# Kernel tuning notes

Measured on AMD Instinct MI355X. Metric: run time of the kernel, lower is better.

The kernel has to match this reference:

```python
import jax, jax.numpy as jnp
import numpy as np

N_NODES = 50000
N_EDGES = 800000
NUM_GRAPHS = 4
IN_DIM, HID_DIM, OUT_DIM = 1024, 128, 1
MAX_RISK = 5.0


def gcn_conv(x, W, b, src, dst, n):
    """PyG GCNConv: add self-loops, sym-normalize, gather-GEMM-scatter."""
    loop = jnp.arange(n, dtype=src.dtype)
    s = jnp.concatenate([src, loop])
    d = jnp.concatenate([dst, loop])
    deg = jax.ops.segment_sum(jnp.ones_like(d, dtype=x.dtype), d, num_segments=n)
    dinv = jnp.where(deg > 0, jax.lax.rsqrt(deg), 0.0)
    norm = dinv[s] * dinv[d]  # [E+N]
    xw = x @ W                # dense GEMM first (fewer FLOPs than per-edge)
    msg = xw[s] * norm[:, None]          # irregular gather, [E+N, out]
    out = jax.ops.segment_sum(msg, d, num_segments=n)  # scatter-add
    return out + b


def setup_inputs() -> dict:
    key = jax.random.key(0)
    ks = jax.random.split(key, 12)
    x = jax.random.normal(ks[0], (N_NODES, IN_DIM), dtype=jnp.float32)
    edge_index = jax.random.randint(ks[1], (2, N_EDGES), 0, N_NODES, dtype=jnp.int64)
    batch = jnp.sort(jax.random.randint(ks[2], (N_NODES,), 0, NUM_GRAPHS, dtype=jnp.int64))

    def glorot(k, fan_in, fan_out):
        s = np.sqrt(6.0 / (fan_in + fan_out)).astype(np.float32)
        return jax.random.uniform(k, (fan_in, fan_out), jnp.float32, -s, s)

    params = {
        'W0': glorot(ks[3], IN_DIM, HID_DIM),  'b0': jnp.zeros((HID_DIM,), jnp.float32),
        'W1': glorot(ks[4], HID_DIM, HID_DIM), 'b1': jnp.zeros((HID_DIM,), jnp.float32),
        'W2': glorot(ks[5], HID_DIM, HID_DIM), 'b2': jnp.zeros((HID_DIM,), jnp.float32),
        'Wl1': glorot(ks[6], 2 * HID_DIM, HID_DIM), 'bl1': jnp.zeros((HID_DIM,), jnp.float32),
        'Wl2': glorot(ks[7], HID_DIM, HID_DIM // 2), 'bl2': jnp.zeros((HID_DIM // 2,), jnp.float32),
        'Wl3': glorot(ks[8], HID_DIM // 2, OUT_DIM), 'bl3': jnp.zeros((OUT_DIM,), jnp.float32),
    }
    return dict(x=x, edge_index=edge_index, batch=batch, **params)


def reference(x, edge_index, batch, W0, b0, W1, b1, W2, b2, Wl1, bl1, Wl2, bl2, Wl3, bl3):
    n = x.shape[0]
    src, dst = edge_index[0], edge_index[1]
    h = jax.nn.relu(gcn_conv(x, W0, b0, src, dst, n))
    h = jax.nn.relu(gcn_conv(h, W1, b1, src, dst, n))
    h = jax.nn.relu(gcn_conv(h, W2, b2, src, dst, n))
    # global max pool + global mean pool per graph
    gmax = jax.ops.segment_max(h, batch, num_segments=NUM_GRAPHS)
    gsum = jax.ops.segment_sum(h, batch, num_segments=NUM_GRAPHS)
    cnt = jax.ops.segment_sum(jnp.ones((n,), h.dtype), batch, num_segments=NUM_GRAPHS)
    gmean = gsum / jnp.maximum(cnt, 1.0)[:, None]
    g = jnp.concatenate([gmax, gmean], axis=1)  # [G, 2*hid]
    g = jax.nn.relu(g @ Wl1 + bl1)
    g = jax.nn.relu(g @ Wl2 + bl2)
    out = g @ Wl3 + bl3
    return jnp.minimum(out, MAX_RISK)
```

## Files before the change

### kernel.cpp

```cpp
#include <hip/hip_runtime.h>
#include <math.h>

#define HID 128
#define NGRAPH 4

typedef int idx_t;
typedef float f32x4 __attribute__((ext_vector_type(4)));
typedef _Float16 h8 __attribute__((ext_vector_type(8)));

__global__ __launch_bounds__(256) void k_count(const idx_t* __restrict__ dst,
                                               int* __restrict__ cnt, int E) {
  int e = blockIdx.x * 256 + threadIdx.x;
  if (e < E) atomicAdd(&cnt[dst[e]], 1);
}

#define SC 1024
__global__ __launch_bounds__(256) void k_scan1(const int* __restrict__ cnt,
                                               int* __restrict__ bsum, int n) {
  __shared__ int sh[256];
  int base = blockIdx.x * SC + threadIdx.x * 4;
  int s = 0;
#pragma unroll
  for (int j = 0; j < 4; ++j) { int i = base + j; if (i < n) s += cnt[i]; }
  sh[threadIdx.x] = s;
  __syncthreads();
  for (int o = 128; o > 0; o >>= 1) {
    if (threadIdx.x < o) sh[threadIdx.x] += sh[threadIdx.x + o];
    __syncthreads();
  }
  if (threadIdx.x == 0) bsum[blockIdx.x] = sh[0];
}

__global__ __launch_bounds__(64) void k_scan2(const int* __restrict__ bsum,
                                              int* __restrict__ boff,
                                              int* __restrict__ off, int nb, int n) {
  int lane = threadIdx.x;
  int v = (lane < nb) ? bsum[lane] : 0;
  for (int d = 1; d < 64; d <<= 1) {
    int t = __shfl_up(v, d);
    if (lane >= d) v += t;
  }
  int ex = __shfl_up(v, 1);
  if (lane == 0) ex = 0;
  if (lane < nb) boff[lane] = ex;
  if (lane == nb - 1) off[n] = v;
}

__global__ __launch_bounds__(256) void k_scan3(const int* __restrict__ cnt,
                                               const int* __restrict__ boff,
                                               int* __restrict__ off,
                                               float* __restrict__ dinv, int n) {
  __shared__ int sh[256];
  int base = blockIdx.x * SC + threadIdx.x * 4;
  int c[4];
  int s = 0;
#pragma unroll
  for (int j = 0; j < 4; ++j) {
    int i = base + j;
    c[j] = (i < n) ? cnt[i] : 0;
    s += c[j];
  }
  sh[threadIdx.x] = s;
  __syncthreads();
  for (int o = 1; o < 256; o <<= 1) {
    int t = (threadIdx.x >= (unsigned)o) ? sh[threadIdx.x - o] : 0;
    __syncthreads();
    sh[threadIdx.x] += t;
    __syncthreads();
  }
  int ex = sh[threadIdx.x] - s + boff[blockIdx.x];
#pragma unroll
  for (int j = 0; j < 4; ++j) {
    int i = base + j;
    if (i < n) {
      off[i] = ex;
      dinv[i] = 1.0f / sqrtf((float)c[j] + 1.0f);
      ex += c[j];
    }
  }
}

__global__ __launch_bounds__(256) void k_fill(const idx_t* __restrict__ src,
                                              const idx_t* __restrict__ dst,
                                              const int* __restrict__ off,
                                              const float* __restrict__ dinv,
                                              int* __restrict__ fillc,
                                              int2* __restrict__ edata, int E) {
  int e = blockIdx.x * 256 + threadIdx.x;
  if (e < E) {
    int s = src[e], d = dst[e];
    int p = atomicAdd(&fillc[d], 1);
    float w = dinv[s] * dinv[d];
    edata[off[d] + p] = make_int2(s, __float_as_int(w));
  }
}

__global__ __launch_bounds__(256) void k_wsplit(const float* __restrict__ W,
                                                _Float16* __restrict__ Wh,
                                                _Float16* __restrict__ Wl, int K) {
  int i = blockIdx.x * 256 + threadIdx.x;
  if (i >= K * HID) return;
  int k = i >> 7, n = i & 127;
  float f = W[i];
  _Float16 h = (_Float16)f;
  Wh[(size_t)n * K + k] = h;
  Wl[(size_t)n * K + k] = (_Float16)(f - (float)h);
}

template <int K, bool F32>
__global__ __launch_bounds__(64) void k_gemm4(const void* __restrict__ Xv,
                                              const _Float16* __restrict__ Wh,
                                              const _Float16* __restrict__ Wl,
                                              _Float16* __restrict__ Y16, int M) {
  const int lane = threadIdx.x & 63;
  const int lrow = lane & 15, kg = lane >> 4;
  const int row0 = blockIdx.x * 32;
  const int ra = row0 + lrow, rb = row0 + 16 + lrow;
  const int rca = (ra < M) ? ra : 0, rcb = (rb < M) ? rb : 0;
  const float* xf0 = (const float*)Xv + (size_t)rca * K + kg * 8;
  const float* xf1 = (const float*)Xv + (size_t)rcb * K + kg * 8;
  const _Float16* xg0 = (const _Float16*)Xv + (size_t)rca * K + kg * 8;
  const _Float16* xg1 = (const _Float16*)Xv + (size_t)rcb * K + kg * 8;
  const _Float16* bh_p = Wh + (size_t)lrow * K + kg * 8;
  const _Float16* bl_p = Wl + (size_t)lrow * K + kg * 8;

  f32x4 acc[2][8] = {};

  for (int k0 = 0; k0 < K; k0 += 32) {
    h8 ah0, al0, ah1, al1;
    if (F32) {
      float4 a0 = *(const float4*)(xf0 + k0);
      float4 a1 = *(const float4*)(xf0 + k0 + 4);
      float4 a2 = *(const float4*)(xf1 + k0);
      float4 a3 = *(const float4*)(xf1 + k0 + 4);
      float t0[8] = {a0.x, a0.y, a0.z, a0.w, a1.x, a1.y, a1.z, a1.w};
      float t1[8] = {a2.x, a2.y, a2.z, a2.w, a3.x, a3.y, a3.z, a3.w};
#pragma unroll
      for (int j = 0; j < 8; ++j) {
        _Float16 h0 = (_Float16)t0[j], h1 = (_Float16)t1[j];
        ah0[j] = h0; al0[j] = (_Float16)(t0[j] - (float)h0);
        ah1[j] = h1; al1[j] = (_Float16)(t1[j] - (float)h1);
      }
    } else {
      ah0 = *(const h8*)(xg0 + k0);
      ah1 = *(const h8*)(xg1 + k0);
    }
#pragma unroll
    for (int ni = 0; ni < 8; ++ni) {
      h8 bh = *(const h8*)(bh_p + (size_t)ni * 16 * K + k0);
      h8 bl = *(const h8*)(bl_p + (size_t)ni * 16 * K + k0);
      acc[0][ni] = __builtin_amdgcn_mfma_f32_16x16x32_f16(ah0, bh, acc[0][ni], 0, 0, 0);
      acc[1][ni] = __builtin_amdgcn_mfma_f32_16x16x32_f16(ah1, bh, acc[1][ni], 0, 0, 0);
      if (F32) {
        acc[0][ni] = __builtin_amdgcn_mfma_f32_16x16x32_f16(al0, bh, acc[0][ni], 0, 0, 0);
        acc[1][ni] = __builtin_amdgcn_mfma_f32_16x16x32_f16(al1, bh, acc[1][ni], 0, 0, 0);
      }
      acc[0][ni] = __builtin_amdgcn_mfma_f32_16x16x32_f16(ah0, bl, acc[0][ni], 0, 0, 0);
      acc[1][ni] = __builtin_amdgcn_mfma_f32_16x16x32_f16(ah1, bl, acc[1][ni], 0, 0, 0);
    }
  }
#pragma unroll
  for (int mi = 0; mi < 2; ++mi)
#pragma unroll
    for (int ni = 0; ni < 8; ++ni)
#pragma unroll
      for (int rr = 0; rr < 4; ++rr) {
        int grow = row0 + mi * 16 + kg * 4 + rr;
        if (grow < M)
          Y16[(size_t)grow * HID + ni * 16 + lrow] = (_Float16)acc[mi][ni][rr];
      }
}

__global__ __launch_bounds__(256) void k_agg16(const _Float16* __restrict__ xh,
                                               const float* __restrict__ dinv,
                                               const int* __restrict__ off,
                                               const int2* __restrict__ edata,
                                               const float* __restrict__ bias,
                                               _Float16* __restrict__ hout, int n) {
  int v = blockIdx.x * 4 + (threadIdx.x >> 6);
  if (v >= n) return;
  int lane = threadIdx.x & 63;
  int grp = lane >> 3, gl = lane & 7;
  int fb = gl * 16;
  float acc[16] = {0.f, 0.f, 0.f, 0.f, 0.f, 0.f, 0.f, 0.f,
                   0.f, 0.f, 0.f, 0.f, 0.f, 0.f, 0.f, 0.f};
  int j0 = off[v], j1 = off[v + 1];
  for (int j = j0 + grp; j < j1; j += 8) {
    int2 e = edata[j];
    float w = __int_as_float(e.y);
    h8 m0 = *(const h8*)&xh[(size_t)e.x * HID + fb];
    h8 m1 = *(const h8*)&xh[(size_t)e.x * HID + fb + 8];
#pragma unroll
    for (int q = 0; q < 8; ++q) {
      acc[q] = fmaf(w, (float)m0[q], acc[q]);
      acc[8 + q] = fmaf(w, (float)m1[q], acc[8 + q]);
    }
  }
#pragma unroll
  for (int q = 0; q < 16; ++q) {
    acc[q] += __shfl_xor(acc[q], 8);
    acc[q] += __shfl_xor(acc[q], 16);
    acc[q] += __shfl_xor(acc[q], 32);
  }
  if (grp == 0) {
    float dv = dinv[v], dv2 = dv * dv;
    h8 s0 = *(const h8*)&xh[(size_t)v * HID + fb];
    h8 s1 = *(const h8*)&xh[(size_t)v * HID + fb + 8];
    h8 o0, o1;
#pragma unroll
    for (int q = 0; q < 8; ++q) {
      float a0 = fmaxf(fmaf(dv2, (float)s0[q], acc[q]) + bias[fb + q], 0.f);
      float a1 = fmaxf(fmaf(dv2, (float)s1[q], acc[8 + q]) + bias[fb + 8 + q], 0.f);
      o0[q] = (_Float16)a0;
      o1[q] = (_Float16)a1;
    }
    *(h8*)&hout[(size_t)v * HID + fb] = o0;
    *(h8*)&hout[(size_t)v * HID + fb + 8] = o1;
  }
}

__global__ __launch_bounds__(256) void k_gcnt(const idx_t* __restrict__ batch,
                                              int* __restrict__ gcnt, int n) {
  __shared__ int h[NGRAPH];
  int tid = threadIdx.x;
  if (tid < NGRAPH) h[tid] = 0;
  __syncthreads();
  int i = blockIdx.x * 256 + tid;
  if (i < n) atomicAdd(&h[batch[i]], 1);
  __syncthreads();
  if (tid < NGRAPH && h[tid]) atomicAdd(&gcnt[tid], h[tid]);
}

__global__ __launch_bounds__(128) void k_pool(const _Float16* __restrict__ h,
                                              const idx_t* __restrict__ batch,
                                              float* __restrict__ gmax,
                                              float* __restrict__ gsum, int n) {
  int f = threadIdx.x;
  int v0 = blockIdx.x * 128;
  int cur = -1;
  float mx = 0.f, sm = 0.f;
  for (int i = 0; i < 128; ++i) {
    int v = v0 + i;
    if (v >= n) break;
    int g = batch[v];
    if (g != cur) {
      if (cur >= 0) {
        atomicMax((int*)&gmax[cur * HID + f], __float_as_int(mx));
        atomicAdd(&gsum[cur * HID + f], sm);
      }
      cur = g; mx = 0.f; sm = 0.f;
    }
    float val = (float)h[(size_t)v * HID + f];
    mx = fmaxf(mx, val);
    sm += val;
  }
  if (cur >= 0) {
    atomicMax((int*)&gmax[cur * HID + f], __float_as_int(mx));
    atomicAdd(&gsum[cur * HID + f], sm);
  }
}

__global__ __launch_bounds__(256) void k_mlp(const float* __restrict__ gmax,
                                             const float* __restrict__ gsum,
                                             const int* __restrict__ gcnt,
                                             const float* __restrict__ Wl1,
                                             const float* __restrict__ bl1,
                                             const float* __restrict__ Wl2,
                                             const float* __restrict__ bl2,
                                             const float* __restrict__ Wl3,
                                             const float* __restrict__ bl3,
                                             float* __restrict__ out) {
  __shared__ float G[NGRAPH][2 * HID];
  __shared__ float H1[NGRAPH][HID];
  __shared__ float H2[NGRAPH][HID / 2];
  int t = threadIdx.x;
  for (int i = t; i < NGRAPH * 2 * HID; i += 256) {
    int gi = i >> 8, j = i & 255;
    float val;
    if (j < HID) val = gmax[gi * HID + j];
    else val = gsum[gi * HID + (j - HID)] / fmaxf((float)gcnt[gi], 1.0f);
    G[gi][j] = val;
  }
  __syncthreads();
  for (int i = t; i < NGRAPH * HID; i += 256) {
    int gi = i >> 7, j = i & 127;
    float a = bl1[j];
    for (int k = 0; k < 2 * HID; ++k) a = fmaf(G[gi][k], Wl1[k * HID + j], a);
    H1[gi][j] = fmaxf(a, 0.f);
  }
  __syncthreads();
  {
    int gi = t >> 6, j = t & 63;
    float a = bl2[j];
    for (int k = 0; k < HID; ++k) a = fmaf(H1[gi][k], Wl2[k * 64 + j], a);
    H2[gi][j] = fmaxf(a, 0.f);
  }
  __syncthreads();
  if (t < NGRAPH) {
    float a = bl3[0];
    for (int k = 0; k < 64; ++k) a = fmaf(H2[t][k], Wl3[k], a);
    out[t] = fminf(a, 5.0f);
  }
}

extern "C" void kernel_launch(void* const* d_in, const int* in_sizes, int n_in,
                              void* d_out, int out_size, void* d_ws, size_t ws_size,
                              hipStream_t stream) {
  const float* x   = (const float*)d_in[0];
  const idx_t* ei  = (const idx_t*)d_in[1];
  const idx_t* bat = (const idx_t*)d_in[2];
  const float* W0 = (const float*)d_in[3];  const float* b0 = (const float*)d_in[4];
  const float* W1 = (const float*)d_in[5];  const float* b1 = (const float*)d_in[6];
  const float* W2 = (const float*)d_in[7];  const float* b2 = (const float*)d_in[8];
  const float* Wl1 = (const float*)d_in[9];  const float* bl1 = (const float*)d_in[10];
  const float* Wl2 = (const float*)d_in[11]; const float* bl2 = (const float*)d_in[12];
  const float* Wl3 = (const float*)d_in[13]; const float* bl3 = (const float*)d_in[14];
  float* out = (float*)d_out;

  const int N = in_sizes[2];
  const int E = in_sizes[1] / 2;
  const idx_t* srcv = ei;
  const idx_t* dstv = ei + E;
  const int nb = (N + SC - 1) / SC;

  char* ws = (char*)d_ws;
  size_t o = 0;
  auto alloc = [&](size_t bytes) -> void* {
    void* p = ws + o;
    o = (o + bytes + 255) & ~(size_t)255;
    return p;
  };
  _Float16* xh  = (_Float16*)alloc((size_t)N * HID * 2);
  _Float16* h16 = (_Float16*)alloc((size_t)N * HID * 2);
  float* dinv = (float*)alloc((size_t)N * 4);
  int* cnt    = (int*)alloc((size_t)N * 4);
  int* off    = (int*)alloc((size_t)(N + 1) * 4);
  int* fillc  = (int*)alloc((size_t)N * 4);
  int2* edata = (int2*)alloc((size_t)E * 8);
  int* bsum   = (int*)alloc(64 * 4);
  int* boff   = (int*)alloc(64 * 4);
  _Float16* Wh0 = (_Float16*)alloc((size_t)1024 * HID * 2);
  _Float16* Wl0 = (_Float16*)alloc((size_t)1024 * HID * 2);
  _Float16* Wh1 = (_Float16*)alloc((size_t)HID * HID * 2);
  _Float16* Wlo1 = (_Float16*)alloc((size_t)HID * HID * 2);
  _Float16* Wh2 = (_Float16*)alloc((size_t)HID * HID * 2);
  _Float16* Wlo2 = (_Float16*)alloc((size_t)HID * HID * 2);
  float* gmax = (float*)alloc(NGRAPH * HID * 4);
  float* gsum = (float*)alloc(NGRAPH * HID * 4);
  int* gcnt   = (int*)alloc(NGRAPH * 4);

  hipMemsetAsync(cnt, 0, (size_t)N * 4, stream);
  hipMemsetAsync(fillc, 0, (size_t)N * 4, stream);
  hipMemsetAsync(gmax, 0, NGRAPH * HID * 4, stream);
  hipMemsetAsync(gsum, 0, NGRAPH * HID * 4, stream);
  hipMemsetAsync(gcnt, 0, NGRAPH * 4, stream);

  k_wsplit<<<(1024 * HID + 255) / 256, 256, 0, stream>>>(W0, Wh0, Wl0, 1024);
  k_wsplit<<<(HID * HID + 255) / 256, 256, 0, stream>>>(W1, Wh1, Wlo1, HID);
  k_wsplit<<<(HID * HID + 255) / 256, 256, 0, stream>>>(W2, Wh2, Wlo2, HID);

  k_count<<<(E + 255) / 256, 256, 0, stream>>>(dstv, cnt, E);
  k_scan1<<<nb, 256, 0, stream>>>(cnt, bsum, N);
  k_scan2<<<1, 64, 0, stream>>>(bsum, boff, off, nb, N);
  k_scan3<<<nb, 256, 0, stream>>>(cnt, boff, off, dinv, N);
  k_fill<<<(E + 255) / 256, 256, 0, stream>>>(srcv, dstv, off, dinv, fillc, edata, E);

  const int gblk = (N + 31) / 32;
  const int ablk = (N + 3) / 4;
  k_gemm4<1024, true><<<gblk, 64, 0, stream>>>(x, Wh0, Wl0, xh, N);
  k_agg16<<<ablk, 256, 0, stream>>>(xh, dinv, off, edata, b0, h16, N);
  k_gemm4<HID, false><<<gblk, 64, 0, stream>>>(h16, Wh1, Wlo1, xh, N);
  k_agg16<<<ablk, 256, 0, stream>>>(xh, dinv, off, edata, b1, h16, N);
  k_gemm4<HID, false><<<gblk, 64, 0, stream>>>(h16, Wh2, Wlo2, xh, N);
  k_agg16<<<ablk, 256, 0, stream>>>(xh, dinv, off, edata, b2, h16, N);

  k_gcnt<<<(N + 255) / 256, 256, 0, stream>>>(bat, gcnt, N);
  k_pool<<<(N + 127) / 128, 128, 0, stream>>>(h16, bat, gmax, gsum, N);
  k_mlp<<<1, 256, 0, stream>>>(gmax, gsum, gcnt, Wl1, bl1, Wl2, bl2, Wl3, bl3, out);
}
```

Before: 451.7 us.

## Split GEMM K across four waves with LDS reduction and fragment-packed weights

The GEMM kernel now uses 256-thread blocks where each of four waves handles a quarter of the K dimension for the same 32-row tile, and the partial sums are combined in shared memory. Weights are pre-packed into MFMA fragment order so each lane's B load is contiguous, and the output is written as 16-byte vector stores. The aim is more parallelism per tile and better-coalesced weight and output traffic. The cost is a serialized four-step LDS reduction with barriers and extra shared-memory use per block.

```diff
diff --git a/kernel.cpp b/kernel.cpp
--- a/kernel.cpp
+++ b/kernel.cpp
@@ -95,44 +95,49 @@
   }
 }
 
-__global__ __launch_bounds__(256) void k_wsplit(const float* __restrict__ W,
-                                                _Float16* __restrict__ Wh,
-                                                _Float16* __restrict__ Wl, int K) {
+__global__ __launch_bounds__(256) void k_wsplitf(const float* __restrict__ W,
+                                                 _Float16* __restrict__ Wh,
+                                                 _Float16* __restrict__ Wl, int K) {
   int i = blockIdx.x * 256 + threadIdx.x;
   if (i >= K * HID) return;
-  int k = i >> 7, n = i & 127;
-  float f = W[i];
+  int j = i & 7, lane = (i >> 3) & 63, ni = (i >> 9) & 7, t = i >> 12;
+  int k = t * 32 + (lane >> 4) * 8 + j;
+  int col = ni * 16 + (lane & 15);
+  float f = W[(size_t)k * HID + col];
   _Float16 h = (_Float16)f;
-  Wh[(size_t)n * K + k] = h;
-  Wl[(size_t)n * K + k] = (_Float16)(f - (float)h);
+  Wh[i] = h;
+  Wl[i] = (_Float16)(f - (float)h);
 }
 
 template <int K, bool F32>
-__global__ __launch_bounds__(64) void k_gemm4(const void* __restrict__ Xv,
-                                              const _Float16* __restrict__ Wh,
-                                              const _Float16* __restrict__ Wl,
-                                              _Float16* __restrict__ Y16, int M) {
-  const int lane = threadIdx.x & 63;
+__global__ __launch_bounds__(256, 4) void k_gemm5(const void* __restrict__ Xv,
+                                                  const _Float16* __restrict__ Wfh,
+                                                  const _Float16* __restrict__ Wfl,
+                                                  _Float16* __restrict__ Y16, int M) {
+  constexpr int KPW = K / 4;
+  constexpr int NT = KPW / 32;
+  const int tid = threadIdx.x;
+  const int wid = tid >> 6, lane = tid & 63;
   const int lrow = lane & 15, kg = lane >> 4;
   const int row0 = blockIdx.x * 32;
   const int ra = row0 + lrow, rb = row0 + 16 + lrow;
   const int rca = (ra < M) ? ra : 0, rcb = (rb < M) ? rb : 0;
-  const float* xf0 = (const float*)Xv + (size_t)rca * K + kg * 8;
-  const float* xf1 = (const float*)Xv + (size_t)rcb * K + kg * 8;
-  const _Float16* xg0 = (const _Float16*)Xv + (size_t)rca * K + kg * 8;
-  const _Float16* xg1 = (const _Float16*)Xv + (size_t)rcb * K + kg * 8;
-  const _Float16* bh_p = Wh + (size_t)lrow * K + kg * 8;
-  const _Float16* bl_p = Wl + (size_t)lrow * K + kg * 8;
+  const float* xf0 = (const float*)Xv + (size_t)rca * K + wid * KPW + kg * 8;
+  const float* xf1 = (const float*)Xv + (size_t)rcb * K + wid * KPW + kg * 8;
+  const _Float16* xg0 = (const _Float16*)Xv + (size_t)rca * K + wid * KPW + kg * 8;
+  const _Float16* xg1 = (const _Float16*)Xv + (size_t)rcb * K + wid * KPW + kg * 8;
 
   f32x4 acc[2][8] = {};
 
-  for (int k0 = 0; k0 < K; k0 += 32) {
+#pragma unroll
+  for (int t = 0; t < NT; ++t) {
+    const int kk = t * 32;
     h8 ah0, al0, ah1, al1;
     if (F32) {
-      float4 a0 = *(const float4*)(xf0 + k0);
-      float4 a1 = *(const float4*)(xf0 + k0 + 4);
-      float4 a2 = *(const float4*)(xf1 + k0);
-      float4 a3 = *(const float4*)(xf1 + k0 + 4);
+      float4 a0 = *(const float4*)(xf0 + kk);
+      float4 a1 = *(const float4*)(xf0 + kk + 4);
+      float4 a2 = *(const float4*)(xf1 + kk);
+      float4 a3 = *(const float4*)(xf1 + kk + 4);
       float t0[8] = {a0.x, a0.y, a0.z, a0.w, a1.x, a1.y, a1.z, a1.w};
       float t1[8] = {a2.x, a2.y, a2.z, a2.w, a3.x, a3.y, a3.z, a3.w};
 #pragma unroll
@@ -142,13 +147,14 @@
         ah1[j] = h1; al1[j] = (_Float16)(t1[j] - (float)h1);
       }
     } else {
-      ah0 = *(const h8*)(xg0 + k0);
-      ah1 = *(const h8*)(xg1 + k0);
-    }
+      ah0 = *(const h8*)(xg0 + kk);
+      ah1 = *(const h8*)(xg1 + kk);
+    }
+    const size_t fb = (size_t)((wid * NT + t) * 8) * 512 + lane * 8;
 #pragma unroll
     for (int ni = 0; ni < 8; ++ni) {
-      h8 bh = *(const h8*)(bh_p + (size_t)ni * 16 * K + k0);
-      h8 bl = *(const h8*)(bl_p + (size_t)ni * 16 * K + k0);
+      h8 bh = *(const h8*)(Wfh + fb + ni * 512);
+      h8 bl = *(const h8*)(Wfl + fb + ni * 512);
       acc[0][ni] = __builtin_amdgcn_mfma_f32_16x16x32_f16(ah0, bh, acc[0][ni], 0, 0, 0);
       acc[1][ni] = __builtin_amdgcn_mfma_f32_16x16x32_f16(ah1, bh, acc[1][ni], 0, 0, 0);
       if (F32) {
@@ -159,16 +165,35 @@
       acc[1][ni] = __builtin_amdgcn_mfma_f32_16x16x32_f16(ah1, bl, acc[1][ni], 0, 0, 0);
     }
   }
-#pragma unroll
-  for (int mi = 0; mi < 2; ++mi)
-#pragma unroll
-    for (int ni = 0; ni < 8; ++ni)
-#pragma unroll
-      for (int rr = 0; rr < 4; ++rr) {
-        int grow = row0 + mi * 16 + kg * 4 + rr;
-        if (grow < M)
-          Y16[(size_t)grow * HID + ni * 16 + lrow] = (_Float16)acc[mi][ni][rr];
-      }
+
+  __shared__ float red[32][132];
+  for (int w = 0; w < 4; ++w) {
+    if (wid == w) {
+#pragma unroll
+      for (int mi = 0; mi < 2; ++mi)
+#pragma unroll
+        for (int ni = 0; ni < 8; ++ni)
+#pragma unroll
+          for (int rr = 0; rr < 4; ++rr) {
+            int r = mi * 16 + kg * 4 + rr, c = ni * 16 + lrow;
+            if (w == 0) red[r][c] = acc[mi][ni][rr];
+            else red[r][c] += acc[mi][ni][rr];
+          }
+    }
+    __syncthreads();
+  }
+  int r = tid >> 3, c0 = (tid & 7) * 16;
+  int grow = row0 + r;
+  if (grow < M) {
+    h8 o0, o1;
+#pragma unroll
+    for (int q = 0; q < 8; ++q) {
+      o0[q] = (_Float16)red[r][c0 + q];
+      o1[q] = (_Float16)red[r][c0 + 8 + q];
+    }
+    *(h8*)&Y16[(size_t)grow * HID + c0] = o0;
+    *(h8*)&Y16[(size_t)grow * HID + c0 + 8] = o1;
+  }
 }
 
 __global__ __launch_bounds__(256) void k_agg16(const _Float16* __restrict__ xh,
@@ -355,9 +380,9 @@
   hipMemsetAsync(gsum, 0, NGRAPH * HID * 4, stream);
   hipMemsetAsync(gcnt, 0, NGRAPH * 4, stream);
 
-  k_wsplit<<<(1024 * HID + 255) / 256, 256, 0, stream>>>(W0, Wh0, Wl0, 1024);
-  k_wsplit<<<(HID * HID + 255) / 256, 256, 0, stream>>>(W1, Wh1, Wlo1, HID);
-  k_wsplit<<<(HID * HID + 255) / 256, 256, 0, stream>>>(W2, Wh2, Wlo2, HID);
+  k_wsplitf<<<(1024 * HID + 255) / 256, 256, 0, stream>>>(W0, Wh0, Wl0, 1024);
+  k_wsplitf<<<(HID * HID + 255) / 256, 256, 0, stream>>>(W1, Wh1, Wlo1, HID);
+  k_wsplitf<<<(HID * HID + 255) / 256, 256, 0, stream>>>(W2, Wh2, Wlo2, HID);
 
   k_count<<<(E + 255) / 256, 256, 0, stream>>>(dstv, cnt, E);
   k_scan1<<<nb, 256, 0, stream>>>(cnt, bsum, N);
@@ -367,11 +392,11 @@
 
   const int gblk = (N + 31) / 32;
   const int ablk = (N + 3) / 4;
-  k_gemm4<1024, true><<<gblk, 64, 0, stream>>>(x, Wh0, Wl0, xh, N);
+  k_gemm5<1024, true><<<gblk, 256, 0, stream>>>(x, Wh0, Wl0, xh, N);
   k_agg16<<<ablk, 256, 0, stream>>>(xh, dinv, off, edata, b0, h16, N);
-  k_gemm4<HID, false><<<gblk, 64, 0, stream>>>(h16, Wh1, Wlo1, xh, N);
+  k_gemm5<HID, false><<<gblk, 256, 0, stream>>>(h16, Wh1, Wlo1, xh, N);
   k_agg16<<<ablk, 256, 0, stream>>>(xh, dinv, off, edata, b1, h16, N);
-  k_gemm4<HID, false><<<gblk, 64, 0, stream>>>(h16, Wh2, Wlo2, xh, N);
+  k_gemm5<HID, false><<<gblk, 256, 0, stream>>>(h16, Wh2, Wlo2, xh, N);
   k_agg16<<<ablk, 256, 0, stream>>>(xh, dinv, off, edata, b2, h16, N);
 
   k_gcnt<<<(N + 255) / 256, 256, 0, stream>>>(bat, gcnt, N);
```

Measured after the change: 371.1 us. -17.9%, faster.
